# Kernel optimization log

Measured on AMD Instinct MI355X. Metric: run time of the kernel, lower is better.

The kernel has to match this reference:

```python
import jax, jax.numpy as jnp
import numpy as np

NEG_SLOPE = 0.01  # jax.nn.leaky_relu default

def bicubic_resize(x, target_h, target_w):
    # NHWC bicubic resize with antialiasing (matches original module)
    b, h, w, c = x.shape
    return jax.image.resize(x, shape=(b, target_h, target_w, c), method='bicubic', antialias=True)

def setup_inputs() -> dict:
    key = jax.random.key(0)
    x = jax.random.normal(key, (16, 128, 128, 128), dtype=jnp.float32)  # NHWC
    return {"x": x, "in_size": 128, "out_size": 128}

def reference(x, in_size, out_size):
    y = bicubic_resize(x, 2 * in_size, 2 * in_size)
    # activation on the fine grid
    y = jax.nn.leaky_relu(y, negative_slope=NEG_SLOPE)
    # downsample (antialiased) back to out_size
    y = bicubic_resize(y, out_size, out_size)
    return y
```

## Files before the change

### kernel.cpp

```cpp
#include <hip/hip_runtime.h>


typedef _Float16 h2 __attribute__((ext_vector_type(2)));

#define HH 128
#define WW 128
#define CC 128
#define RS 16
#define CH 16
#define PADH2 132
#define NSTEP (RS + 4)

#define LBAR() asm volatile("s_waitcnt lgkmcnt(0)\n\ts_barrier" ::: "memory")

__device__ __forceinline__ h2 H2(float v) {
  _Float16 h = (_Float16)v;
  return (h2){h, h};
}

__device__ __forceinline__ double keys_cubic(double x) {
  if (x >= 2.0) return 0.0;
  if (x >= 1.0) return ((-0.5 * x + 2.5) * x - 4.0) * x + 2.0;
  return (1.5 * x - 2.5) * x * x + 1.0;
}

__global__ __launch_bounds__(256) void fused_updown_kernel(
    const float* __restrict__ x, float* __restrict__ out) {
  __shared__ __align__(16) float wUpV[256][4];
  __shared__ __align__(16) float wDnE[4][8];
  __shared__ __align__(16) h2 wUpH2[6][4];
  __shared__ __align__(16) h2 wDnH2[4][8];
  __shared__ __align__(16) h2 rowv[2][CH][PADH2];

  const int tid = threadIdx.x;

  {
    const int k = tid;
    const double q = 0.5 * k - 0.25;
    const int st = ((k + 1) >> 1) - 2;
    double wr[4], s = 0.0;
#pragma unroll
    for (int i = 0; i < 4; ++i) {
      const int col = st + i;
      double w = (col >= 0 && col <= 127) ? keys_cubic(fabs((double)col - q)) : 0.0;
      wr[i] = w; s += w;
    }
    const double inv = 1.0 / s;
#pragma unroll
    for (int i = 0; i < 4; ++i) wUpV[k][i] = (float)(wr[i] * inv);
  }
  if (tid < 4) {
    const int e = tid;
    const int j = (e < 2) ? e : 124 + e;
    const double p = 2.0 * j + 0.5;
    const int st = 2 * j - 3;
    double wr[8], s = 0.0;
#pragma unroll
    for (int i = 0; i < 8; ++i) {
      const int col = st + i;
      double w = (col >= 0 && col <= 255) ? keys_cubic(0.5 * fabs((double)col - p)) : 0.0;
      wr[i] = w; s += w;
    }
    const double inv = 1.0 / s;
#pragma unroll
    for (int i = 0; i < 8; ++i) wDnE[e][i] = (float)(wr[i] * inv);
  }
  __syncthreads();
  if (tid < 6) {
    const int k = (tid < 3) ? tid : 250 + tid;
#pragma unroll
    for (int i = 0; i < 4; ++i) wUpH2[tid][i] = H2(wUpV[k][i]);
  }
  if (tid < 4) {
#pragma unroll
    for (int i = 0; i < 8; ++i) wDnH2[tid][i] = H2(wDnE[tid][i]);
  }

  const int bid = blockIdx.x;
  const int b = bid & 15;
  const int strip = (bid >> 4) & 7;
  const int chunk = bid >> 7;
  const int oy0 = strip * RS;
  const int c0 = chunk * CH;
  const int c = tid & 15;
  const int g = tid >> 4;
  const int col0 = g * 8;
  const bool gL = (g == 0), gR = (g == 15);

  const float* xbase = x + (size_t)b * (HH * WW * CC) + (size_t)col0 * CC + (c0 + c);
  float* obase = out + (size_t)b * (HH * WW * CC) + (size_t)col0 * CC + (c0 + c);
  const int m0 = oy0 - 2;

  auto load_row = [&](float (&d)[8], int row) {
    row = row < 0 ? 0 : (row > 127 ? 127 : row);
    const float* p = xbase + (size_t)row * (WW * CC);
#pragma unroll
    for (int j = 0; j < 8; ++j) d[j] = p[j * CC];
  };

  auto wdGet = [&](int oy, float cst, int tap) -> float {
    if (oy < 0 || oy > 127) return 0.f;
    if (oy < 2) return wDnE[oy][tap];
    if (oy > 125) return wDnE[oy - 124][tap];
    return cst;
  };

  float r0[8], r1[8], r2[8], r3[8], r4[8], r5[8];
  float A0[8], A1[8], A2[8], A3[8], A4[8];
#pragma unroll
  for (int i = 0; i < 8; ++i) { A0[i]=0.f; A1[i]=0.f; A2[i]=0.f; A3[i]=0.f; A4[i]=0.f; }

  load_row(r0, m0 - 2);
  load_row(r1, m0 - 1);
  load_row(r2, m0);
  load_row(r3, m0 + 1);
  load_row(r4, m0 + 2);
  load_row(r5, m0 + 3);

  for (int t = 0; t < NSTEP; ++t) {
    const int m = m0 + t;
    if (t > 0) {
#pragma unroll
      for (int i = 0; i < 8; ++i) {
        r0[i]=r1[i]; r1[i]=r2[i]; r2[i]=r3[i]; r3[i]=r4[i]; r4[i]=r5[i];
      }
      load_row(r5, m + 3);
    }
    const bool mOK = (m >= 0) && (m <= 127);
    const int sp = t & 1;
    __align__(16) h2 vh[8];
    if (mOK) {
      float4 we, wo;
      if (m >= 2 && m <= 125) {
        we = make_float4(-0.0234375f, 0.2265625f, 0.8671875f, -0.0703125f);
        wo = make_float4(-0.0703125f, 0.8671875f, 0.2265625f, -0.0234375f);
      } else {
        we = *(const float4*)wUpV[2 * m];
        wo = *(const float4*)wUpV[2 * m + 1];
      }
#pragma unroll
      for (int j = 0; j < 8; ++j) {
        const float vE = (we.x * r0[j] + we.y * r1[j]) + (we.z * r2[j] + we.w * r3[j]);
        const float vO = (wo.x * r1[j] + wo.y * r2[j]) + (wo.z * r3[j] + wo.w * r4[j]);
        vh[j] = (h2){(_Float16)vE, (_Float16)vO};
      }
      *(float4*)&rowv[sp][c][col0]     = *(const float4*)&vh[0];
      *(float4*)&rowv[sp][c][col0 + 4] = *(const float4*)&vh[4];
    }
    LBAR();
    if (mOK) {
      __align__(16) h2 vv[16];
      if (!gL) {
        *(float4*)&vv[0] = *(const float4*)&rowv[sp][c][col0 - 4];
      } else {
#pragma unroll
        for (int i = 0; i < 4; ++i) vv[i] = H2(0.f);
      }
#pragma unroll
      for (int j = 0; j < 8; ++j) vv[4 + j] = vh[j];
      if (!gR) {
        *(float4*)&vv[12] = *(const float4*)&rowv[sp][c][col0 + 8];
      } else {
#pragma unroll
        for (int i = 0; i < 4; ++i) vv[12 + i] = H2(0.f);
      }

      h2 ff[22];
#pragma unroll
      for (int u = 0; u < 22; ++u) {
        const int s = (u >> 1) + 1;
        h2 t2;
        if (u & 1)
          t2 = (vv[s] * H2(-0.0234375f) + vv[s + 1] * H2(0.2265625f))
             + (vv[s + 2] * H2(0.8671875f) + vv[s + 3] * H2(-0.0703125f));
        else
          t2 = (vv[s] * H2(-0.0703125f) + vv[s + 1] * H2(0.8671875f))
             + (vv[s + 2] * H2(0.2265625f) + vv[s + 3] * H2(-0.0234375f));
        ff[u] = __builtin_elementwise_max(t2, t2 * H2(0.01f));
      }
      if (gL) {
#pragma unroll
        for (int u = 3; u <= 5; ++u) {
          const int s = (u >> 1) + 1;
          h2 t2 = (vv[s] * wUpH2[u - 3][0] + vv[s + 1] * wUpH2[u - 3][1])
                + (vv[s + 2] * wUpH2[u - 3][2] + vv[s + 3] * wUpH2[u - 3][3]);
          ff[u] = __builtin_elementwise_max(t2, t2 * H2(0.01f));
        }
      }
      if (gR) {
#pragma unroll
        for (int u = 16; u <= 18; ++u) {
          const int s = (u >> 1) + 1;
          h2 t2 = (vv[s] * wUpH2[u - 13][0] + vv[s + 1] * wUpH2[u - 13][1])
                + (vv[s + 2] * wUpH2[u - 13][2] + vv[s + 3] * wUpH2[u - 13][3]);
          ff[u] = __builtin_elementwise_max(t2, t2 * H2(0.01f));
        }
      }

      h2 tt[8];
#pragma unroll
      for (int jj = 0; jj < 8; ++jj) {
        const h2 p0 = ff[2*jj]     + ff[2*jj + 7];
        const h2 p1 = ff[2*jj + 1] + ff[2*jj + 6];
        const h2 p2 = ff[2*jj + 2] + ff[2*jj + 5];
        const h2 p3 = ff[2*jj + 3] + ff[2*jj + 4];
        tt[jj] = (p0 * H2(-0.01171875f) + p1 * H2(-0.03515625f))
               + (p2 * H2(0.11328125f)  + p3 * H2(0.43359375f));
      }
      if (gL) {
#pragma unroll
        for (int jj = 0; jj < 2; ++jj) {
          h2 s2 = H2(0.f);
#pragma unroll
          for (int i = 0; i < 8; ++i) s2 += ff[2*jj + i] * wDnH2[jj][i];
          tt[jj] = s2;
        }
      }
      if (gR) {
#pragma unroll
        for (int jj = 6; jj < 8; ++jj) {
          h2 s2 = H2(0.f);
#pragma unroll
          for (int i = 0; i < 8; ++i) s2 += ff[2*jj + i] * wDnH2[jj - 4][i];
          tt[jj] = s2;
        }
      }

      const float wE0 = wdGet(m - 2, -0.01171875f, 7);
      const float wE1 = wdGet(m - 1, 0.11328125f, 5);
      const float wE2 = wdGet(m, 0.43359375f, 3);
      const float wE3 = wdGet(m + 1, -0.03515625f, 1);
      const float wO0 = wdGet(m - 1, -0.03515625f, 6);
      const float wO1 = wdGet(m, 0.43359375f, 4);
      const float wO2 = wdGet(m + 1, 0.11328125f, 2);
      const float wO3 = wdGet(m + 2, -0.01171875f, 0);
#pragma unroll
      for (int jj = 0; jj < 8; ++jj) {
        const float te = (float)tt[jj].x, to = (float)tt[jj].y;
        A0[jj] = fmaf(wE0, te, A0[jj]);
        A1[jj] = fmaf(wE1, te, fmaf(wO0, to, A1[jj]));
        A2[jj] = fmaf(wE2, te, fmaf(wO1, to, A2[jj]));
        A3[jj] = fmaf(wE3, te, fmaf(wO2, to, A3[jj]));
        A4[jj] = fmaf(wO3, to, A4[jj]);
      }
    }
    if (m - 2 >= oy0) {
      float* op = obase + (size_t)(m - 2) * (WW * CC);
#pragma unroll
      for (int jj = 0; jj < 8; ++jj) op[jj * CC] = A0[jj];
    }
#pragma unroll
    for (int jj = 0; jj < 8; ++jj) {
      A0[jj]=A1[jj]; A1[jj]=A2[jj]; A2[jj]=A3[jj]; A3[jj]=A4[jj]; A4[jj]=0.f;
    }
  }
}

extern "C" void kernel_launch(void* const* d_in, const int* in_sizes, int n_in,
                              void* d_out, int out_size, void* d_ws, size_t ws_size,
                              hipStream_t stream) {
  const float* x = (const float*)d_in[0];
  float* o = (float*)d_out;
  dim3 grid(16 * 8 * 8);
  dim3 block(256);
  hipLaunchKernelGGL(fused_updown_kernel, grid, block, 0, stream, x, o);
}
```

Before: 96.03 us.

## Replace LDS halo exchange and barrier with direct global halo loads

Each thread now loads 14 input columns per row (its 8 columns plus a clamped halo of 3 on each side) directly from global memory. It recomputes the vertical upsample for those halo columns itself instead of exchanging them through shared memory, which removes the per-row LDS store/load and block barrier. This costs redundant global loads (mostly expected to hit cache), extra vertical-pass arithmetic and higher register pressure. The row-ahead prefetch is also shortened, so load latency is less hidden. The fp16 weight setup is folded into the first init phase, dropping one post-barrier pass.

```diff
diff --git a/kernel.cpp b/kernel.cpp
--- a/kernel.cpp
+++ b/kernel.cpp
@@ -8,10 +8,8 @@
 #define CC 128
 #define RS 16
 #define CH 16
-#define PADH2 132
+#define NC 14
 #define NSTEP (RS + 4)
-
-#define LBAR() asm volatile("s_waitcnt lgkmcnt(0)\n\ts_barrier" ::: "memory")
 
 __device__ __forceinline__ h2 H2(float v) {
   _Float16 h = (_Float16)v;
@@ -30,7 +28,6 @@
   __shared__ __align__(16) float wDnE[4][8];
   __shared__ __align__(16) h2 wUpH2[6][4];
   __shared__ __align__(16) h2 wDnH2[4][8];
-  __shared__ __align__(16) h2 rowv[2][CH][PADH2];
 
   const int tid = threadIdx.x;
 
@@ -48,6 +45,21 @@
     const double inv = 1.0 / s;
 #pragma unroll
     for (int i = 0; i < 4; ++i) wUpV[k][i] = (float)(wr[i] * inv);
+  }
+  if (tid < 6) {
+    const int k = (tid < 3) ? tid : 250 + tid;
+    const double q = 0.5 * k - 0.25;
+    const int st = ((k + 1) >> 1) - 2;
+    double wr[4], s = 0.0;
+#pragma unroll
+    for (int i = 0; i < 4; ++i) {
+      const int col = st + i;
+      double w = (col >= 0 && col <= 127) ? keys_cubic(fabs((double)col - q)) : 0.0;
+      wr[i] = w; s += w;
+    }
+    const double inv = 1.0 / s;
+#pragma unroll
+    for (int i = 0; i < 4; ++i) wUpH2[tid][i] = H2((float)(wr[i] * inv));
   }
   if (tid < 4) {
     const int e = tid;
@@ -63,18 +75,13 @@
     }
     const double inv = 1.0 / s;
 #pragma unroll
-    for (int i = 0; i < 8; ++i) wDnE[e][i] = (float)(wr[i] * inv);
+    for (int i = 0; i < 8; ++i) {
+      const float wf = (float)(wr[i] * inv);
+      wDnE[e][i] = wf;
+      wDnH2[e][i] = H2(wf);
+    }
   }
   __syncthreads();
-  if (tid < 6) {
-    const int k = (tid < 3) ? tid : 250 + tid;
-#pragma unroll
-    for (int i = 0; i < 4; ++i) wUpH2[tid][i] = H2(wUpV[k][i]);
-  }
-  if (tid < 4) {
-#pragma unroll
-    for (int i = 0; i < 8; ++i) wDnH2[tid][i] = H2(wDnE[tid][i]);
-  }
 
   const int bid = blockIdx.x;
   const int b = bid & 15;
@@ -87,15 +94,22 @@
   const int col0 = g * 8;
   const bool gL = (g == 0), gR = (g == 15);
 
-  const float* xbase = x + (size_t)b * (HH * WW * CC) + (size_t)col0 * CC + (c0 + c);
+  int co[NC];
+#pragma unroll
+  for (int i = 0; i < NC; ++i) {
+    int cl = col0 - 3 + i;
+    cl = cl < 0 ? 0 : (cl > 127 ? 127 : cl);
+    co[i] = cl * CC;
+  }
+  const float* xb = x + (size_t)b * (HH * WW * CC) + (c0 + c);
   float* obase = out + (size_t)b * (HH * WW * CC) + (size_t)col0 * CC + (c0 + c);
   const int m0 = oy0 - 2;
 
-  auto load_row = [&](float (&d)[8], int row) {
+  auto ldrow = [&](float (&d)[NC], int row) {
     row = row < 0 ? 0 : (row > 127 ? 127 : row);
-    const float* p = xbase + (size_t)row * (WW * CC);
-#pragma unroll
-    for (int j = 0; j < 8; ++j) d[j] = p[j * CC];
+    const float* p = xb + (size_t)row * (WW * CC);
+#pragma unroll
+    for (int i = 0; i < NC; ++i) d[i] = p[co[i]];
   };
 
   auto wdGet = [&](int oy, float cst, int tap) -> float {
@@ -105,30 +119,24 @@
     return cst;
   };
 
-  float r0[8], r1[8], r2[8], r3[8], r4[8], r5[8];
+  float R0[NC], R1[NC], R2[NC], R3[NC], R4[NC];
   float A0[8], A1[8], A2[8], A3[8], A4[8];
 #pragma unroll
   for (int i = 0; i < 8; ++i) { A0[i]=0.f; A1[i]=0.f; A2[i]=0.f; A3[i]=0.f; A4[i]=0.f; }
 
-  load_row(r0, m0 - 2);
-  load_row(r1, m0 - 1);
-  load_row(r2, m0);
-  load_row(r3, m0 + 1);
-  load_row(r4, m0 + 2);
-  load_row(r5, m0 + 3);
+  ldrow(R0, m0 - 2);
+  ldrow(R1, m0 - 1);
+  ldrow(R2, m0);
+  ldrow(R3, m0 + 1);
 
   for (int t = 0; t < NSTEP; ++t) {
     const int m = m0 + t;
     if (t > 0) {
 #pragma unroll
-      for (int i = 0; i < 8; ++i) {
-        r0[i]=r1[i]; r1[i]=r2[i]; r2[i]=r3[i]; r3[i]=r4[i]; r4[i]=r5[i];
-      }
-      load_row(r5, m + 3);
-    }
+      for (int i = 0; i < NC; ++i) { R0[i]=R1[i]; R1[i]=R2[i]; R2[i]=R3[i]; R3[i]=R4[i]; }
+    }
+    ldrow(R4, m + 2);
     const bool mOK = (m >= 0) && (m <= 127);
-    const int sp = t & 1;
-    __align__(16) h2 vh[8];
     if (mOK) {
       float4 we, wo;
       if (m >= 2 && m <= 125) {
@@ -138,61 +146,42 @@
         we = *(const float4*)wUpV[2 * m];
         wo = *(const float4*)wUpV[2 * m + 1];
       }
-#pragma unroll
-      for (int j = 0; j < 8; ++j) {
-        const float vE = (we.x * r0[j] + we.y * r1[j]) + (we.z * r2[j] + we.w * r3[j]);
-        const float vO = (wo.x * r1[j] + wo.y * r2[j]) + (wo.z * r3[j] + wo.w * r4[j]);
-        vh[j] = (h2){(_Float16)vE, (_Float16)vO};
-      }
-      *(float4*)&rowv[sp][c][col0]     = *(const float4*)&vh[0];
-      *(float4*)&rowv[sp][c][col0 + 4] = *(const float4*)&vh[4];
-    }
-    LBAR();
-    if (mOK) {
-      __align__(16) h2 vv[16];
-      if (!gL) {
-        *(float4*)&vv[0] = *(const float4*)&rowv[sp][c][col0 - 4];
-      } else {
-#pragma unroll
-        for (int i = 0; i < 4; ++i) vv[i] = H2(0.f);
-      }
-#pragma unroll
-      for (int j = 0; j < 8; ++j) vv[4 + j] = vh[j];
-      if (!gR) {
-        *(float4*)&vv[12] = *(const float4*)&rowv[sp][c][col0 + 8];
-      } else {
-#pragma unroll
-        for (int i = 0; i < 4; ++i) vv[12 + i] = H2(0.f);
+      h2 vvn[NC];
+#pragma unroll
+      for (int i = 0; i < NC; ++i) {
+        const float vE = (we.x * R0[i] + we.y * R1[i]) + (we.z * R2[i] + we.w * R3[i]);
+        const float vO = (wo.x * R1[i] + wo.y * R2[i]) + (wo.z * R3[i] + wo.w * R4[i]);
+        vvn[i] = (h2){(_Float16)vE, (_Float16)vO};
       }
 
       h2 ff[22];
 #pragma unroll
       for (int u = 0; u < 22; ++u) {
-        const int s = (u >> 1) + 1;
+        const int s = u >> 1;
         h2 t2;
         if (u & 1)
-          t2 = (vv[s] * H2(-0.0234375f) + vv[s + 1] * H2(0.2265625f))
-             + (vv[s + 2] * H2(0.8671875f) + vv[s + 3] * H2(-0.0703125f));
+          t2 = (vvn[s] * H2(-0.0234375f) + vvn[s + 1] * H2(0.2265625f))
+             + (vvn[s + 2] * H2(0.8671875f) + vvn[s + 3] * H2(-0.0703125f));
         else
-          t2 = (vv[s] * H2(-0.0703125f) + vv[s + 1] * H2(0.8671875f))
-             + (vv[s + 2] * H2(0.2265625f) + vv[s + 3] * H2(-0.0234375f));
+          t2 = (vvn[s] * H2(-0.0703125f) + vvn[s + 1] * H2(0.8671875f))
+             + (vvn[s + 2] * H2(0.2265625f) + vvn[s + 3] * H2(-0.0234375f));
         ff[u] = __builtin_elementwise_max(t2, t2 * H2(0.01f));
       }
       if (gL) {
 #pragma unroll
         for (int u = 3; u <= 5; ++u) {
-          const int s = (u >> 1) + 1;
-          h2 t2 = (vv[s] * wUpH2[u - 3][0] + vv[s + 1] * wUpH2[u - 3][1])
-                + (vv[s + 2] * wUpH2[u - 3][2] + vv[s + 3] * wUpH2[u - 3][3]);
+          const int s = u >> 1;
+          h2 t2 = (vvn[s] * wUpH2[u - 3][0] + vvn[s + 1] * wUpH2[u - 3][1])
+                + (vvn[s + 2] * wUpH2[u - 3][2] + vvn[s + 3] * wUpH2[u - 3][3]);
           ff[u] = __builtin_elementwise_max(t2, t2 * H2(0.01f));
         }
       }
       if (gR) {
 #pragma unroll
         for (int u = 16; u <= 18; ++u) {
-          const int s = (u >> 1) + 1;
-          h2 t2 = (vv[s] * wUpH2[u - 13][0] + vv[s + 1] * wUpH2[u - 13][1])
-                + (vv[s + 2] * wUpH2[u - 13][2] + vv[s + 3] * wUpH2[u - 13][3]);
+          const int s = u >> 1;
+          h2 t2 = (vvn[s] * wUpH2[u - 13][0] + vvn[s + 1] * wUpH2[u - 13][1])
+                + (vvn[s + 2] * wUpH2[u - 13][2] + vvn[s + 3] * wUpH2[u - 13][3]);
           ff[u] = __builtin_elementwise_max(t2, t2 * H2(0.01f));
         }
       }
```

After: 110.7 us. +15.2%, slower.

## Rotate row and accumulator registers via 5-way unrolled step macro and use fdot2

Applied to the files above, without the earlier changes.

Replaces the shifting sliding window of row and accumulator registers with a 5-way unrolled loop that rotates register names, so the per-step register copies go away. This drops one row buffer by issuing the next row load into the slot just consumed, after the horizontal pass and before the barrier. Interior rows accumulate the vertical downsample with packed fp16 dot2 instructions instead of separate float FMAs. The cost is larger unrolled code, a slight change in accumulation precision, and a load issued later than before.

```diff
diff --git a/kernel.cpp b/kernel.cpp
--- a/kernel.cpp
+++ b/kernel.cpp
@@ -91,7 +91,7 @@
   float* obase = out + (size_t)b * (HH * WW * CC) + (size_t)col0 * CC + (c0 + c);
   const int m0 = oy0 - 2;
 
-  auto load_row = [&](float (&d)[8], int row) {
+  auto ldrow = [&](float (&d)[8], int row) {
     row = row < 0 ? 0 : (row > 127 ? 127 : row);
     const float* p = xbase + (size_t)row * (WW * CC);
 #pragma unroll
@@ -105,155 +105,149 @@
     return cst;
   };
 
-  float r0[8], r1[8], r2[8], r3[8], r4[8], r5[8];
+  const h2 WDA = (h2){(_Float16)(-0.01171875f), (_Float16)(0.f)};
+  const h2 WDB = (h2){(_Float16)(0.11328125f), (_Float16)(-0.03515625f)};
+  const h2 WDC = (h2){(_Float16)(0.43359375f), (_Float16)(0.43359375f)};
+  const h2 WDD = (h2){(_Float16)(-0.03515625f), (_Float16)(0.11328125f)};
+  const h2 WDE = (h2){(_Float16)(0.f), (_Float16)(-0.01171875f)};
+
+  float R0[8], R1[8], R2[8], R3[8], R4[8];
   float A0[8], A1[8], A2[8], A3[8], A4[8];
 #pragma unroll
   for (int i = 0; i < 8; ++i) { A0[i]=0.f; A1[i]=0.f; A2[i]=0.f; A3[i]=0.f; A4[i]=0.f; }
 
-  load_row(r0, m0 - 2);
-  load_row(r1, m0 - 1);
-  load_row(r2, m0);
-  load_row(r3, m0 + 1);
-  load_row(r4, m0 + 2);
-  load_row(r5, m0 + 3);
-
-  for (int t = 0; t < NSTEP; ++t) {
-    const int m = m0 + t;
-    if (t > 0) {
-#pragma unroll
-      for (int i = 0; i < 8; ++i) {
-        r0[i]=r1[i]; r1[i]=r2[i]; r2[i]=r3[i]; r3[i]=r4[i]; r4[i]=r5[i];
-      }
-      load_row(r5, m + 3);
-    }
-    const bool mOK = (m >= 0) && (m <= 127);
-    const int sp = t & 1;
-    __align__(16) h2 vh[8];
-    if (mOK) {
-      float4 we, wo;
-      if (m >= 2 && m <= 125) {
-        we = make_float4(-0.0234375f, 0.2265625f, 0.8671875f, -0.0703125f);
-        wo = make_float4(-0.0703125f, 0.8671875f, 0.2265625f, -0.0234375f);
-      } else {
-        we = *(const float4*)wUpV[2 * m];
-        wo = *(const float4*)wUpV[2 * m + 1];
-      }
-#pragma unroll
-      for (int j = 0; j < 8; ++j) {
-        const float vE = (we.x * r0[j] + we.y * r1[j]) + (we.z * r2[j] + we.w * r3[j]);
-        const float vO = (wo.x * r1[j] + wo.y * r2[j]) + (wo.z * r3[j] + wo.w * r4[j]);
-        vh[j] = (h2){(_Float16)vE, (_Float16)vO};
-      }
-      *(float4*)&rowv[sp][c][col0]     = *(const float4*)&vh[0];
-      *(float4*)&rowv[sp][c][col0 + 4] = *(const float4*)&vh[4];
-    }
-    LBAR();
-    if (mOK) {
-      __align__(16) h2 vv[16];
-      if (!gL) {
-        *(float4*)&vv[0] = *(const float4*)&rowv[sp][c][col0 - 4];
-      } else {
-#pragma unroll
-        for (int i = 0; i < 4; ++i) vv[i] = H2(0.f);
-      }
-#pragma unroll
-      for (int j = 0; j < 8; ++j) vv[4 + j] = vh[j];
-      if (!gR) {
-        *(float4*)&vv[12] = *(const float4*)&rowv[sp][c][col0 + 8];
-      } else {
-#pragma unroll
-        for (int i = 0; i < 4; ++i) vv[12 + i] = H2(0.f);
-      }
-
-      h2 ff[22];
-#pragma unroll
-      for (int u = 0; u < 22; ++u) {
-        const int s = (u >> 1) + 1;
-        h2 t2;
-        if (u & 1)
-          t2 = (vv[s] * H2(-0.0234375f) + vv[s + 1] * H2(0.2265625f))
-             + (vv[s + 2] * H2(0.8671875f) + vv[s + 3] * H2(-0.0703125f));
-        else
-          t2 = (vv[s] * H2(-0.0703125f) + vv[s + 1] * H2(0.8671875f))
-             + (vv[s + 2] * H2(0.2265625f) + vv[s + 3] * H2(-0.0234375f));
-        ff[u] = __builtin_elementwise_max(t2, t2 * H2(0.01f));
-      }
-      if (gL) {
-#pragma unroll
-        for (int u = 3; u <= 5; ++u) {
-          const int s = (u >> 1) + 1;
-          h2 t2 = (vv[s] * wUpH2[u - 3][0] + vv[s + 1] * wUpH2[u - 3][1])
-                + (vv[s + 2] * wUpH2[u - 3][2] + vv[s + 3] * wUpH2[u - 3][3]);
-          ff[u] = __builtin_elementwise_max(t2, t2 * H2(0.01f));
-        }
-      }
-      if (gR) {
-#pragma unroll
-        for (int u = 16; u <= 18; ++u) {
-          const int s = (u >> 1) + 1;
-          h2 t2 = (vv[s] * wUpH2[u - 13][0] + vv[s + 1] * wUpH2[u - 13][1])
-                + (vv[s + 2] * wUpH2[u - 13][2] + vv[s + 3] * wUpH2[u - 13][3]);
-          ff[u] = __builtin_elementwise_max(t2, t2 * H2(0.01f));
-        }
-      }
-
-      h2 tt[8];
-#pragma unroll
-      for (int jj = 0; jj < 8; ++jj) {
-        const h2 p0 = ff[2*jj]     + ff[2*jj + 7];
-        const h2 p1 = ff[2*jj + 1] + ff[2*jj + 6];
-        const h2 p2 = ff[2*jj + 2] + ff[2*jj + 5];
-        const h2 p3 = ff[2*jj + 3] + ff[2*jj + 4];
-        tt[jj] = (p0 * H2(-0.01171875f) + p1 * H2(-0.03515625f))
-               + (p2 * H2(0.11328125f)  + p3 * H2(0.43359375f));
-      }
-      if (gL) {
-#pragma unroll
-        for (int jj = 0; jj < 2; ++jj) {
-          h2 s2 = H2(0.f);
-#pragma unroll
-          for (int i = 0; i < 8; ++i) s2 += ff[2*jj + i] * wDnH2[jj][i];
-          tt[jj] = s2;
-        }
-      }
-      if (gR) {
-#pragma unroll
-        for (int jj = 6; jj < 8; ++jj) {
-          h2 s2 = H2(0.f);
-#pragma unroll
-          for (int i = 0; i < 8; ++i) s2 += ff[2*jj + i] * wDnH2[jj - 4][i];
-          tt[jj] = s2;
-        }
-      }
-
-      const float wE0 = wdGet(m - 2, -0.01171875f, 7);
-      const float wE1 = wdGet(m - 1, 0.11328125f, 5);
-      const float wE2 = wdGet(m, 0.43359375f, 3);
-      const float wE3 = wdGet(m + 1, -0.03515625f, 1);
-      const float wO0 = wdGet(m - 1, -0.03515625f, 6);
-      const float wO1 = wdGet(m, 0.43359375f, 4);
-      const float wO2 = wdGet(m + 1, 0.11328125f, 2);
-      const float wO3 = wdGet(m + 2, -0.01171875f, 0);
-#pragma unroll
-      for (int jj = 0; jj < 8; ++jj) {
-        const float te = (float)tt[jj].x, to = (float)tt[jj].y;
-        A0[jj] = fmaf(wE0, te, A0[jj]);
-        A1[jj] = fmaf(wE1, te, fmaf(wO0, to, A1[jj]));
-        A2[jj] = fmaf(wE2, te, fmaf(wO1, to, A2[jj]));
-        A3[jj] = fmaf(wE3, te, fmaf(wO2, to, A3[jj]));
-        A4[jj] = fmaf(wO3, to, A4[jj]);
-      }
-    }
-    if (m - 2 >= oy0) {
-      float* op = obase + (size_t)(m - 2) * (WW * CC);
-#pragma unroll
-      for (int jj = 0; jj < 8; ++jj) op[jj * CC] = A0[jj];
-    }
-#pragma unroll
-    for (int jj = 0; jj < 8; ++jj) {
-      A0[jj]=A1[jj]; A1[jj]=A2[jj]; A2[jj]=A3[jj]; A3[jj]=A4[jj]; A4[jj]=0.f;
-    }
-  }
+  ldrow(R0, m0 - 2);
+  ldrow(R1, m0 - 1);
+  ldrow(R2, m0);
+  ldrow(R3, m0 + 1);
+  ldrow(R4, m0 + 2);
+
+#define STEP(T_, Ra,Rb,Rc,Rd,Re, Aa,Ab,Ac,Ad,Ae) do {                          \
+    const int m = m0 + (T_);                                                   \
+    const bool mOK = (m >= 0) && (m <= 127);                                   \
+    const int sp = (T_) & 1;                                                   \
+    __align__(16) h2 vh[8];                                                    \
+    if (mOK) {                                                                 \
+      float4 we, wo;                                                           \
+      if (m >= 2 && m <= 125) {                                                \
+        we = make_float4(-0.0234375f, 0.2265625f, 0.8671875f, -0.0703125f);    \
+        wo = make_float4(-0.0703125f, 0.8671875f, 0.2265625f, -0.0234375f);    \
+      } else {                                                                 \
+        we = *(const float4*)wUpV[2 * m];                                      \
+        wo = *(const float4*)wUpV[2 * m + 1];                                  \
+      }                                                                        \
+      _Pragma("unroll") for (int j = 0; j < 8; ++j) {                          \
+        const float vE = (we.x*Ra[j] + we.y*Rb[j]) + (we.z*Rc[j] + we.w*Rd[j]);\
+        const float vO = (wo.x*Rb[j] + wo.y*Rc[j]) + (wo.z*Rd[j] + wo.w*Re[j]);\
+        vh[j] = (h2){(_Float16)vE, (_Float16)vO};                              \
+      }                                                                        \
+      *(float4*)&rowv[sp][c][col0]     = *(const float4*)&vh[0];               \
+      *(float4*)&rowv[sp][c][col0 + 4] = *(const float4*)&vh[4];               \
+    }                                                                          \
+    ldrow(Ra, m + 3);                      \
+    LBAR();                                                                    \
+    if (mOK) {                                                                 \
+      __align__(16) h2 vv[16];                                                 \
+      if (!gL) { *(float4*)&vv[0] = *(const float4*)&rowv[sp][c][col0 - 4]; }  \
+      else { _Pragma("unroll") for (int i = 0; i < 4; ++i) vv[i] = H2(0.f); }  \
+      _Pragma("unroll") for (int j = 0; j < 8; ++j) vv[4 + j] = vh[j];         \
+      if (!gR) { *(float4*)&vv[12] = *(const float4*)&rowv[sp][c][col0 + 8]; } \
+      else { _Pragma("unroll") for (int i = 0; i < 4; ++i) vv[12+i] = H2(0.f);}\
+      h2 ff[22];                                                               \
+      _Pragma("unroll") for (int u = 0; u < 22; ++u) {                         \
+        const int s = (u >> 1) + 1;                                            \
+        h2 t2;                                                                 \
+        if (u & 1)                                                             \
+          t2 = (vv[s] * H2(-0.0234375f) + vv[s + 1] * H2(0.2265625f))          \
+             + (vv[s + 2] * H2(0.8671875f) + vv[s + 3] * H2(-0.0703125f));     \
+        else                                                                   \
+          t2 = (vv[s] * H2(-0.0703125f) + vv[s + 1] * H2(0.8671875f))          \
+             + (vv[s + 2] * H2(0.2265625f) + vv[s + 3] * H2(-0.0234375f));     \
+        ff[u] = __builtin_elementwise_max(t2, t2 * H2(0.01f));                 \
+      }                                                                        \
+      if (gL) {                                                                \
+        _Pragma("unroll") for (int u = 3; u <= 5; ++u) {                       \
+          const int s = (u >> 1) + 1;                                          \
+          h2 t2 = (vv[s] * wUpH2[u-3][0] + vv[s+1] * wUpH2[u-3][1])            \
+                + (vv[s+2] * wUpH2[u-3][2] + vv[s+3] * wUpH2[u-3][3]);         \
+          ff[u] = __builtin_elementwise_max(t2, t2 * H2(0.01f));               \
+        }                                                                      \
+      }                                                                        \
+      if (gR) {                                                                \
+        _Pragma("unroll") for (int u = 16; u <= 18; ++u) {                     \
+          const int s = (u >> 1) + 1;                                          \
+          h2 t2 = (vv[s] * wUpH2[u-13][0] + vv[s+1] * wUpH2[u-13][1])          \
+                + (vv[s+2] * wUpH2[u-13][2] + vv[s+3] * wUpH2[u-13][3]);       \
+          ff[u] = __builtin_elementwise_max(t2, t2 * H2(0.01f));               \
+        }                                                                      \
+      }                                                                        \
+      h2 tt[8];                                                                \
+      _Pragma("unroll") for (int jj = 0; jj < 8; ++jj) {                       \
+        const h2 p0 = ff[2*jj]     + ff[2*jj + 7];                             \
+        const h2 p1 = ff[2*jj + 1] + ff[2*jj + 6];                             \
+        const h2 p2 = ff[2*jj + 2] + ff[2*jj + 5];                             \
+        const h2 p3 = ff[2*jj + 3] + ff[2*jj + 4];                             \
+        tt[jj] = (p0 * H2(-0.01171875f) + p1 * H2(-0.03515625f))               \
+               + (p2 * H2(0.11328125f)  + p3 * H2(0.43359375f));               \
+      }                                                                        \
+      if (gL) {                                                                \
+        _Pragma("unroll") for (int jj = 0; jj < 2; ++jj) {                     \
+          h2 s2 = H2(0.f);                                                     \
+          _Pragma("unroll") for (int i = 0; i < 8; ++i)                        \
+            s2 += ff[2*jj + i] * wDnH2[jj][i];                                 \
+          tt[jj] = s2;                                                         \
+        }                                                                      \
+      }                                                                        \
+      if (gR) {                                                                \
+        _Pragma("unroll") for (int jj = 6; jj < 8; ++jj) {                     \
+          h2 s2 = H2(0.f);                                                     \
+          _Pragma("unroll") for (int i = 0; i < 8; ++i)                        \
+            s2 += ff[2*jj + i] * wDnH2[jj - 4][i];                             \
+          tt[jj] = s2;                                                         \
+        }                                                                      \
+      }                                                                        \
+      if (m >= 4 && m <= 123) {            \
+        _Pragma("unroll") for (int jj = 0; jj < 8; ++jj) {                     \
+          Aa[jj] = __builtin_amdgcn_fdot2(tt[jj], WDA, Aa[jj], false);         \
+          Ab[jj] = __builtin_amdgcn_fdot2(tt[jj], WDB, Ab[jj], false);         \
+          Ac[jj] = __builtin_amdgcn_fdot2(tt[jj], WDC, Ac[jj], false);         \
+          Ad[jj] = __builtin_amdgcn_fdot2(tt[jj], WDD, Ad[jj], false);         \
+          Ae[jj] = __builtin_amdgcn_fdot2(tt[jj], WDE, Ae[jj], false);         \
+        }                                                                      \
+      } else {                          \
+        const float wE0 = wdGet(m - 2, -0.01171875f, 7);                       \
+        const float wE1 = wdGet(m - 1, 0.11328125f, 5);                        \
+        const float wE2 = wdGet(m,     0.43359375f, 3);                        \
+        const float wE3 = wdGet(m + 1, -0.03515625f, 1);                       \
+        const float wO0 = wdGet(m - 1, -0.03515625f, 6);                       \
+        const float wO1 = wdGet(m,     0.43359375f, 4);                        \
+        const float wO2 = wdGet(m + 1, 0.11328125f, 2);                        \
+        const float wO3 = wdGet(m + 2, -0.01171875f, 0);                       \
+        _Pragma("unroll") for (int jj = 0; jj < 8; ++jj) {                     \
+          const float te = (float)tt[jj].x, to = (float)tt[jj].y;              \
+          Aa[jj] = fmaf(wE0, te, Aa[jj]);                                      \
+          Ab[jj] = fmaf(wE1, te, fmaf(wO0, to, Ab[jj]));                       \
+          Ac[jj] = fmaf(wE2, te, fmaf(wO1, to, Ac[jj]));                       \
+          Ad[jj] = fmaf(wE3, te, fmaf(wO2, to, Ad[jj]));                       \
+          Ae[jj] = fmaf(wO3, to, Ae[jj]);                                      \
+        }                                                                      \
+      }                                                                        \
+    }                                                                          \
+    if (m - 2 >= oy0) {                                                        \
+      float* op = obase + (size_t)(m - 2) * (WW * CC);                         \
+      _Pragma("unroll") for (int jj = 0; jj < 8; ++jj) op[jj * CC] = Aa[jj];   \
+    }                                                                          \
+    _Pragma("unroll") for (int jj = 0; jj < 8; ++jj) Aa[jj] = 0.f;             \
+  } while (0)
+
+  for (int tb = 0; tb < NSTEP; tb += 5) {
+    STEP(tb + 0, R0,R1,R2,R3,R4, A0,A1,A2,A3,A4);
+    STEP(tb + 1, R1,R2,R3,R4,R0, A1,A2,A3,A4,A0);
+    STEP(tb + 2, R2,R3,R4,R0,R1, A2,A3,A4,A0,A1);
+    STEP(tb + 3, R3,R4,R0,R1,R2, A3,A4,A0,A1,A2);
+    STEP(tb + 4, R4,R0,R1,R2,R3, A4,A0,A1,A2,A3);
+  }
+#undef STEP
 }
 
 extern "C" void kernel_launch(void* const* d_in, const int* in_sizes, int n_in,
```

New measurement: 96.02 us. No clear change (-0.0%).
